# Kernel tuning notes

Hardware: AMD Instinct MI355X
Metric: run time of the kernel (lower is better)

Reference implementation:

```python
import jax, jax.numpy as jnp
import numpy as np

B, T, D = 2, 2048, 1024
P, ALPHA, P_R = 512, 4, 64
HID = 16 * D
EPS = 1e-6


def rmsnorm(x, w):
    norm = jnp.sqrt(jnp.mean(x * x, axis=-1, keepdims=True) + EPS)
    return x * w / norm


def ssm_lowrank(t, F, b_r, c_r):
    # gated elementwise recurrence h_t = F_t * h_{t-1} + t_t, then low-rank correction
    Fs = jnp.moveaxis(F, 1, 0)   # (T,B,P)
    ts = jnp.moveaxis(t, 1, 0)   # (T,B,P)

    def step(h, inp):
        f, u = inp
        h = f * h + u
        return h, h

    h0 = jnp.zeros((t.shape[0], t.shape[2]), dtype=t.dtype)
    _, hs = jax.lax.scan(step, h0, (Fs, ts))
    h = jnp.moveaxis(hs, 0, 1)   # (B,T,P)
    t_tilde = t + jnp.einsum('btp,pr,rq->btq', h, b_r, c_r)
    return t_tilde


def setup_inputs() -> dict:
    key = jax.random.key(0)
    ks = jax.random.split(key, 11)
    s = lambda fan: 1.0 / np.sqrt(fan)
    return {
        'x':       jax.random.normal(ks[0], (B, T, D), jnp.float32),
        'w_norm1': jnp.ones((D,), jnp.float32),
        'w_toP':   jax.random.normal(ks[1], (D, P), jnp.float32) * s(D),
        'w_emb':   jax.random.normal(ks[2], (D, ALPHA * P), jnp.float32) * s(D),
        'w_f':     jax.random.normal(ks[3], (D, P), jnp.float32) * s(D),
        'b_r':     jax.random.normal(ks[4], (P, P_R), jnp.float32) * s(P),
        'c_r':     jax.random.normal(ks[5], (P_R, P), jnp.float32) * s(P_R),
        'w_fromP': jax.random.normal(ks[6], (P, D), jnp.float32) * s(P),
        'w_norm2': jnp.ones((D,), jnp.float32),
        'w_fc1':   jax.random.normal(ks[7], (D, HID), jnp.float32) * s(D),
        'w_fc2':   jax.random.normal(ks[8], (HID, D), jnp.float32) * s(HID),
    }


def reference(x, w_norm1, w_toP, w_emb, w_f, b_r, c_r, w_fromP, w_norm2, w_fc1, w_fc2):
    # ---- pre-LN CEPTA context path ----
    h1 = rmsnorm(x, w_norm1)
    pre_path = jnp.einsum('btd,dp->btp', h1, w_toP)                 # to_P
    U = jnp.einsum('btd,dk->btk', h1, w_emb).reshape(B, T, ALPHA, P)  # cepta_dense U
    Fgate = jax.nn.sigmoid(jnp.einsum('btd,dp->btp', h1, w_f))      # cepta_dense F
    Y = jax.nn.gelu(U)                                              # cepta_dense Y
    t = jnp.sum(Y, axis=2) + pre_path                               # router reduce='sum'
    t_tilde = ssm_lowrank(t, Fgate, b_r, c_r)                       # low-rank SSM
    y = jnp.einsum('btp,pd->btd', t_tilde, w_fromP)                 # from_P
    x = x + y
    # ---- pre-LN GELU MLP ----
    h2 = rmsnorm(x, w_norm2)
    z = jnp.einsum('bth,hd->btd', jax.nn.gelu(jnp.einsum('btd,dh->bth', h2, w_fc1)), w_fc2)
    return x + z
```

## Files before the change

### kernel.cpp

```cpp
#include <hip/hip_runtime.h>

typedef unsigned short u16;
typedef __bf16 bf16x8 __attribute__((ext_vector_type(8)));
typedef float f32x4 __attribute__((ext_vector_type(4)));
typedef int i32x4 __attribute__((ext_vector_type(4)));

__device__ inline u16 f2bf(float f) {
  union { float f; unsigned u; } v; v.f = f;
  unsigned u = v.u;
  unsigned r = (u + 0x7FFFu + ((u >> 16) & 1u)) >> 16;
  return (u16)r;
}

__device__ inline float gelu_f(float x) {
  float t = 0.7978845608028654f * (x + 0.044715f * x * x * x);
  float a = __expf(-2.f * fabsf(t));
  float th = (1.f - a) / (1.f + a);
  th = copysignf(th, t);
  return 0.5f * x * (1.f + th);
}
__device__ inline float sigmoid_f(float x) { return 1.f / (1.f + __expf(-x)); }

__global__ void transpose_cvt(const float* __restrict__ in, u16* __restrict__ out,
                              int R, int C, int ldout) {
  __shared__ float tile[32][33];
  int c0 = blockIdx.x * 32, r0 = blockIdx.y * 32;
  int tx = threadIdx.x, ty = threadIdx.y;
#pragma unroll
  for (int i = 0; i < 32; i += 8) {
    int r = r0 + ty + i, c = c0 + tx;
    tile[ty + i][tx] = (r < R && c < C) ? in[(long)r * C + c] : 0.f;
  }
  __syncthreads();
#pragma unroll
  for (int i = 0; i < 32; i += 8) {
    int cc = c0 + ty + i, rr = r0 + tx;
    if (cc < C && rr < R) out[(long)cc * ldout + rr] = f2bf(tile[tx][ty + i]);
  }
}

__global__ __launch_bounds__(256) void rmsnorm_k(const float* __restrict__ x,
                                                 const float* __restrict__ w,
                                                 u16* __restrict__ out) {
  int row = blockIdx.x;
  int tid = threadIdx.x;
  const float4* xv = (const float4*)(x + (long)row * 1024);
  float4 v = xv[tid];
  float ss = v.x * v.x + v.y * v.y + v.z * v.z + v.w * v.w;
#pragma unroll
  for (int off = 32; off > 0; off >>= 1) ss += __shfl_down(ss, off);
  __shared__ float red[4];
  if ((tid & 63) == 0) red[tid >> 6] = ss;
  __syncthreads();
  float tot = red[0] + red[1] + red[2] + red[3];
  float scale = rsqrtf(tot * (1.f / 1024.f) + 1e-6f);
  const float4* wv4 = (const float4*)w;
  float4 wv = wv4[tid];
  ushort4 o;
  o.x = f2bf(v.x * wv.x * scale);
  o.y = f2bf(v.y * wv.y * scale);
  o.z = f2bf(v.z * wv.z * scale);
  o.w = f2bf(v.w * wv.w * scale);
  *((ushort4*)(out + (long)row * 1024) + tid) = o;
}

#define EPI_BF16 0
#define EPI_ROUTE1 1
#define EPI_ADD_BF16 2
#define EPI_ADD_F32 3
#define EPI_GELU_BF16 4

template <int EPI>
__global__ __launch_bounds__(256) void gemm_bt(
    const u16* __restrict__ A, const u16* __restrict__ Bt,
    u16* __restrict__ obf, float* __restrict__ of32, const float* __restrict__ add,
    float* __restrict__ og, float* __restrict__ ofl,
    int N, int K, int lda, int ldb) {
  __shared__ __align__(16) u16 As[128 * 64];
  __shared__ __align__(16) u16 Bs[128 * 64];
  const int tid = threadIdx.x;
  const int lane = tid & 63;
  const int wave = tid >> 6;
  const int wm = wave >> 1, wn = wave & 1;
  const int bm0 = blockIdx.y * 128, bn0 = blockIdx.x * 128;

  f32x4 acc[4][4];
  f32x4 zero = {0.f, 0.f, 0.f, 0.f};
#pragma unroll
  for (int m = 0; m < 4; ++m)
#pragma unroll
    for (int n = 0; n < 4; ++n) acc[m][n] = zero;

  i32x4 ra[4], rb[4];
  int srow[4], schk[4];
#pragma unroll
  for (int i = 0; i < 4; ++i) {
    int s = tid + 256 * i;
    srow[i] = s >> 3;
    schk[i] = s & 7;
  }

#pragma unroll
  for (int i = 0; i < 4; ++i) {
    ra[i] = *(const i32x4*)(A + (bm0 + srow[i]) * lda + schk[i] * 8);
    rb[i] = *(const i32x4*)(Bt + (bn0 + srow[i]) * ldb + schk[i] * 8);
  }

  const int nk = K >> 6;
  for (int t = 0; t < nk; ++t) {
#pragma unroll
    for (int i = 0; i < 4; ++i) {
      *(i32x4*)&As[srow[i] * 64 + ((schk[i] ^ (srow[i] & 7)) << 3)] = ra[i];
      *(i32x4*)&Bs[srow[i] * 64 + ((schk[i] ^ (srow[i] & 7)) << 3)] = rb[i];
    }
    __syncthreads();
    if (t + 1 < nk) {
      int k0 = (t + 1) << 6;
#pragma unroll
      for (int i = 0; i < 4; ++i) {
        ra[i] = *(const i32x4*)(A + (bm0 + srow[i]) * lda + k0 + schk[i] * 8);
        rb[i] = *(const i32x4*)(Bt + (bn0 + srow[i]) * ldb + k0 + schk[i] * 8);
      }
    }
#pragma unroll
    for (int kk = 0; kk < 2; ++kk) {
      bf16x8 av[4], bv[4];
#pragma unroll
      for (int m = 0; m < 4; ++m) {
        int r = wm * 64 + m * 16 + (lane & 15);
        int c = kk * 4 + (lane >> 4);
        i32x4 v = *(const i32x4*)&As[r * 64 + ((c ^ (r & 7)) << 3)];
        av[m] = __builtin_bit_cast(bf16x8, v);
      }
#pragma unroll
      for (int n = 0; n < 4; ++n) {
        int r = wn * 64 + n * 16 + (lane & 15);
        int c = kk * 4 + (lane >> 4);
        i32x4 v = *(const i32x4*)&Bs[r * 64 + ((c ^ (r & 7)) << 3)];
        bv[n] = __builtin_bit_cast(bf16x8, v);
      }
#pragma unroll
      for (int m = 0; m < 4; ++m)
#pragma unroll
        for (int n = 0; n < 4; ++n)
          acc[m][n] = __builtin_amdgcn_mfma_f32_16x16x32_bf16(av[m], bv[n], acc[m][n], 0, 0, 0);
    }
    __syncthreads();
  }

#pragma unroll
  for (int m = 0; m < 4; ++m) {
    int row_b = bm0 + wm * 64 + m * 16 + ((lane >> 4) << 2);
#pragma unroll
    for (int n = 0; n < 4; ++n) {
      int col = bn0 + wn * 64 + n * 16 + (lane & 15);
#pragma unroll
      for (int j = 0; j < 4; ++j) {
        int row = row_b + j;
        float v = acc[m][n][j];
        if constexpr (EPI == EPI_BF16) {
          obf[(long)row * N + col] = f2bf(v);
        } else if constexpr (EPI == EPI_ROUTE1) {
          if (col < 512) of32[(long)row * 512 + col] = v;
          else if (col < 2560) og[(long)row * 2048 + (col - 512)] = gelu_f(v);
          else ofl[(long)row * 512 + (col - 2560)] = sigmoid_f(v);
        } else if constexpr (EPI == EPI_ADD_BF16) {
          long idx = (long)row * N + col;
          obf[idx] = f2bf(add[idx] + v);
        } else if constexpr (EPI == EPI_ADD_F32) {
          long idx = (long)row * N + col;
          of32[idx] = add[idx] + v;
        } else {
          obf[(long)row * N + col] = f2bf(gelu_f(v));
        }
      }
    }
  }
}

__global__ __launch_bounds__(256) void router_k(float* __restrict__ tb, const float* __restrict__ G) {
  int i = blockIdx.x * 256 + threadIdx.x;
  int r = i >> 7, pq = i & 127;
  float4 t = ((float4*)tb)[i];
#pragma unroll
  for (int a = 0; a < 4; ++a) {
    float4 g = *((const float4*)(G + (long)r * 2048 + a * 512) + pq);
    t.x += g.x; t.y += g.y; t.z += g.z; t.w += g.w;
  }
  ((float4*)tb)[i] = t;
}

__global__ void scan_chunk(const float* __restrict__ tb, const float* __restrict__ F,
                           float* __restrict__ abuf, float* __restrict__ ubuf) {
  int b = blockIdx.x >> 5, c = blockIdx.x & 31, pidx = threadIdx.x;
  const float* fp = F + ((long)(b * 2048 + c * 64) * 512) + pidx;
  const float* up = tb + ((long)(b * 2048 + c * 64) * 512) + pidx;
  float A = 1.f, U = 0.f;
#pragma unroll 8
  for (int s = 0; s < 64; ++s) {
    float f = fp[(long)s * 512], u = up[(long)s * 512];
    A = f * A;
    U = f * U + u;
  }
  abuf[(b * 32 + c) * 512 + pidx] = A;
  ubuf[(b * 32 + c) * 512 + pidx] = U;
}

__global__ void scan_combine(const float* __restrict__ abuf, const float* __restrict__ ubuf,
                             float* __restrict__ hstart) {
  int b = blockIdx.x, pidx = threadIdx.x;
  float h = 0.f;
  for (int c = 0; c < 32; ++c) {
    hstart[(b * 32 + c) * 512 + pidx] = h;
    h = abuf[(b * 32 + c) * 512 + pidx] * h + ubuf[(b * 32 + c) * 512 + pidx];
  }
}

__global__ void scan_apply(const float* __restrict__ tb, const float* __restrict__ F,
                           const float* __restrict__ hstart, u16* __restrict__ hbf) {
  int b = blockIdx.x >> 5, c = blockIdx.x & 31, pidx = threadIdx.x;
  const float* fp = F + ((long)(b * 2048 + c * 64) * 512) + pidx;
  const float* up = tb + ((long)(b * 2048 + c * 64) * 512) + pidx;
  u16* op = hbf + ((long)(b * 2048 + c * 64) * 512) + pidx;
  float h = hstart[(b * 32 + c) * 512 + pidx];
#pragma unroll 8
  for (int s = 0; s < 64; ++s) {
    float f = fp[(long)s * 512], u = up[(long)s * 512];
    h = f * h + u;
    op[(long)s * 512] = f2bf(h);
  }
}

extern "C" void kernel_launch(void* const* d_in, const int* in_sizes, int n_in,
                              void* d_out, int out_size, void* d_ws, size_t ws_size,
                              hipStream_t stream) {
  const float* x       = (const float*)d_in[0];
  const float* w_norm1 = (const float*)d_in[1];
  const float* w_toP   = (const float*)d_in[2];
  const float* w_emb   = (const float*)d_in[3];
  const float* w_f     = (const float*)d_in[4];
  const float* b_r     = (const float*)d_in[5];
  const float* c_r     = (const float*)d_in[6];
  const float* w_fromP = (const float*)d_in[7];
  const float* w_norm2 = (const float*)d_in[8];
  const float* w_fc1   = (const float*)d_in[9];
  const float* w_fc2   = (const float*)d_in[10];
  float* out = (float*)d_out;

  char* base = (char*)d_ws;
  size_t off = 0;
  auto alloc = [&](size_t bytes) {
    void* r = base + off;
    off += (bytes + 255) & ~(size_t)255;
    return r;
  };
  u16* W1T     = (u16*)alloc((size_t)3072 * 1024 * 2);
  u16* WfromPT = (u16*)alloc((size_t)1024 * 512 * 2);
  u16* Wfc1T   = (u16*)alloc((size_t)16384 * 1024 * 2);
  u16* Wfc2T   = (u16*)alloc((size_t)1024 * 16384 * 2);
  u16* BrT     = (u16*)alloc((size_t)128 * 512 * 2);
  u16* CrT     = (u16*)alloc((size_t)512 * 128 * 2);
  u16* h1      = (u16*)alloc((size_t)4096 * 1024 * 2);
  float* G     = (float*)alloc((size_t)4096 * 2048 * 4);
  float* F     = (float*)alloc((size_t)4096 * 512 * 4);
  float* tb    = (float*)alloc((size_t)4096 * 512 * 4);
  float* abuf  = (float*)alloc((size_t)2 * 32 * 512 * 4);
  float* ubuf  = (float*)alloc((size_t)2 * 32 * 512 * 4);
  float* hstart= (float*)alloc((size_t)2 * 32 * 512 * 4);
  u16* hbf     = (u16*)alloc((size_t)4096 * 512 * 2);
  u16* g1buf   = (u16*)alloc((size_t)4096 * 128 * 2);
  u16* tt      = (u16*)alloc((size_t)4096 * 512 * 2);
  float* xmid  = (float*)alloc((size_t)4096 * 1024 * 4);
  u16* h2      = (u16*)alloc((size_t)4096 * 1024 * 2);
  u16* a3      = (u16*)alloc((size_t)4096 * 4096 * 2);
  (void)ws_size; (void)in_sizes; (void)n_in; (void)out_size;

  dim3 tpb(32, 8);
  transpose_cvt<<<dim3(16, 32), tpb, 0, stream>>>(w_toP, W1T, 1024, 512, 1024);
  transpose_cvt<<<dim3(64, 32), tpb, 0, stream>>>(w_emb, W1T + (size_t)512 * 1024, 1024, 2048, 1024);
  transpose_cvt<<<dim3(16, 32), tpb, 0, stream>>>(w_f, W1T + (size_t)2560 * 1024, 1024, 512, 1024);
  transpose_cvt<<<dim3(32, 16), tpb, 0, stream>>>(w_fromP, WfromPT, 512, 1024, 512);
  transpose_cvt<<<dim3(512, 32), tpb, 0, stream>>>(w_fc1, Wfc1T, 1024, 16384, 1024);
  transpose_cvt<<<dim3(32, 512), tpb, 0, stream>>>(w_fc2, Wfc2T, 16384, 1024, 16384);
  hipMemsetAsync(BrT, 0, (size_t)128 * 512 * 2, stream);
  hipMemsetAsync(CrT, 0, (size_t)512 * 128 * 2, stream);
  transpose_cvt<<<dim3(2, 16), tpb, 0, stream>>>(b_r, BrT, 512, 64, 512);
  transpose_cvt<<<dim3(16, 2), tpb, 0, stream>>>(c_r, CrT, 64, 512, 128);

  rmsnorm_k<<<4096, 256, 0, stream>>>(x, w_norm1, h1);

  gemm_bt<EPI_ROUTE1><<<dim3(24, 32), 256, 0, stream>>>(h1, W1T, nullptr, tb, nullptr, G, F,
                                                        3072, 1024, 1024, 1024);
  router_k<<<2048, 256, 0, stream>>>(tb, G);

  scan_chunk<<<64, 512, 0, stream>>>(tb, F, abuf, ubuf);
  scan_combine<<<2, 512, 0, stream>>>(abuf, ubuf, hstart);
  scan_apply<<<64, 512, 0, stream>>>(tb, F, hstart, hbf);

  gemm_bt<EPI_BF16><<<dim3(1, 32), 256, 0, stream>>>(hbf, BrT, g1buf, nullptr, nullptr, nullptr, nullptr,
                                                     128, 512, 512, 512);
  gemm_bt<EPI_ADD_BF16><<<dim3(4, 32), 256, 0, stream>>>(g1buf, CrT, tt, nullptr, tb, nullptr, nullptr,
                                                         512, 128, 128, 128);
  gemm_bt<EPI_ADD_F32><<<dim3(8, 32), 256, 0, stream>>>(tt, WfromPT, nullptr, xmid, x, nullptr, nullptr,
                                                        1024, 512, 512, 512);
  rmsnorm_k<<<4096, 256, 0, stream>>>(xmid, w_norm2, h2);

  for (int c = 0; c < 4; ++c) {
    gemm_bt<EPI_GELU_BF16><<<dim3(32, 32), 256, 0, stream>>>(
        h2, Wfc1T + (size_t)c * 4096 * 1024, a3, nullptr, nullptr, nullptr, nullptr,
        4096, 1024, 1024, 1024);
    gemm_bt<EPI_ADD_F32><<<dim3(8, 32), 256, 0, stream>>>(
        a3, Wfc2T + (size_t)c * 4096, nullptr, out, (c == 0 ? xmid : out), nullptr, nullptr,
        1024, 4096, 4096, 16384);
  }
}
```

Measured before the change: 597.8 us.

## Use direct global-to-LDS loads, XCD-aware block remap, and split-K for fc2

Replaces the register-staged, XOR-swizzled LDS fill with global_load_lds direct copies, which removes the register prefetch of the next tile and the swizzle, so LDS reads may now hit bank conflicts. It remaps workgroup IDs so consecutive tiles spread across XCDs for better L2 locality. The fc2 GEMM becomes a 2-way split-K writing partial sums into scratch, followed by a separate reduce kernel that adds the residual. This raises parallelism for the 256-block GEMM at the cost of extra fp32 traffic and an additional launch per chunk.

```diff
diff --git a/kernel.cpp b/kernel.cpp
--- a/kernel.cpp
+++ b/kernel.cpp
@@ -20,6 +20,11 @@
   return 0.5f * x * (1.f + th);
 }
 __device__ inline float sigmoid_f(float x) { return 1.f / (1.f + __expf(-x)); }
+
+__device__ __forceinline__ void gld16(const u16* g, u16* l) {
+  __builtin_amdgcn_global_load_lds((const __attribute__((address_space(1))) void*)g,
+                                   (__attribute__((address_space(3))) void*)l, 16, 0, 0);
+}
 
 __global__ void transpose_cvt(const float* __restrict__ in, u16* __restrict__ out,
                               int R, int C, int ldout) {
@@ -69,6 +74,7 @@
 #define EPI_ADD_BF16 2
 #define EPI_ADD_F32 3
 #define EPI_GELU_BF16 4
+#define EPI_PART 5
 
 template <int EPI>
 __global__ __launch_bounds__(256) void gemm_bt(
@@ -81,8 +87,19 @@
   const int tid = threadIdx.x;
   const int lane = tid & 63;
   const int wave = tid >> 6;
+
+  const int gx = gridDim.x, gy = gridDim.y, gz = gridDim.z;
+  const int nwg = gx * gy * gz;
+  int orig = (blockIdx.z * gy + blockIdx.y) * gx + blockIdx.x;
+  int id = ((nwg & 7) == 0) ? ((orig & 7) * (nwg >> 3) + (orig >> 3)) : orig;
+  const int bx = id % gx;
+  const int by = (id / gx) % gy;
+  const int bz = id / (gx * gy);
+
   const int wm = wave >> 1, wn = wave & 1;
-  const int bm0 = blockIdx.y * 128, bn0 = blockIdx.x * 128;
+  const int bm0 = by * 128, bn0 = bx * 128;
+  const int kper = K / gz;
+  const int koff = bz * kper;
 
   f32x4 acc[4][4];
   f32x4 zero = {0.f, 0.f, 0.f, 0.f};
@@ -91,37 +108,19 @@
 #pragma unroll
     for (int n = 0; n < 4; ++n) acc[m][n] = zero;
 
-  i32x4 ra[4], rb[4];
-  int srow[4], schk[4];
-#pragma unroll
-  for (int i = 0; i < 4; ++i) {
-    int s = tid + 256 * i;
-    srow[i] = s >> 3;
-    schk[i] = s & 7;
-  }
-
-#pragma unroll
-  for (int i = 0; i < 4; ++i) {
-    ra[i] = *(const i32x4*)(A + (bm0 + srow[i]) * lda + schk[i] * 8);
-    rb[i] = *(const i32x4*)(Bt + (bn0 + srow[i]) * ldb + schk[i] * 8);
-  }
-
-  const int nk = K >> 6;
+  const int lrow = lane >> 3, lchk = lane & 7;
+  const long abase = (long)(bm0 + wave * 8 + lrow) * lda + koff + lchk * 8;
+  const long bbase = (long)(bn0 + wave * 8 + lrow) * ldb + koff + lchk * 8;
+
+  const int nk = kper >> 6;
   for (int t = 0; t < nk; ++t) {
-#pragma unroll
-    for (int i = 0; i < 4; ++i) {
-      *(i32x4*)&As[srow[i] * 64 + ((schk[i] ^ (srow[i] & 7)) << 3)] = ra[i];
-      *(i32x4*)&Bs[srow[i] * 64 + ((schk[i] ^ (srow[i] & 7)) << 3)] = rb[i];
+    const int k0 = t << 6;
+#pragma unroll
+    for (int j = 0; j < 4; ++j) {
+      gld16(A + abase + (long)j * 32 * lda + k0, &As[(wave * 8 + j * 32) * 64]);
+      gld16(Bt + bbase + (long)j * 32 * ldb + k0, &Bs[(wave * 8 + j * 32) * 64]);
     }
     __syncthreads();
-    if (t + 1 < nk) {
-      int k0 = (t + 1) << 6;
-#pragma unroll
-      for (int i = 0; i < 4; ++i) {
-        ra[i] = *(const i32x4*)(A + (bm0 + srow[i]) * lda + k0 + schk[i] * 8);
-        rb[i] = *(const i32x4*)(Bt + (bn0 + srow[i]) * ldb + k0 + schk[i] * 8);
-      }
-    }
 #pragma unroll
     for (int kk = 0; kk < 2; ++kk) {
       bf16x8 av[4], bv[4];
@@ -129,15 +128,13 @@
       for (int m = 0; m < 4; ++m) {
         int r = wm * 64 + m * 16 + (lane & 15);
         int c = kk * 4 + (lane >> 4);
-        i32x4 v = *(const i32x4*)&As[r * 64 + ((c ^ (r & 7)) << 3)];
-        av[m] = __builtin_bit_cast(bf16x8, v);
+        av[m] = __builtin_bit_cast(bf16x8, *(const i32x4*)&As[r * 64 + c * 8]);
       }
 #pragma unroll
       for (int n = 0; n < 4; ++n) {
         int r = wn * 64 + n * 16 + (lane & 15);
         int c = kk * 4 + (lane >> 4);
-        i32x4 v = *(const i32x4*)&Bs[r * 64 + ((c ^ (r & 7)) << 3)];
-        bv[n] = __builtin_bit_cast(bf16x8, v);
+        bv[n] = __builtin_bit_cast(bf16x8, *(const i32x4*)&Bs[r * 64 + c * 8]);
       }
 #pragma unroll
       for (int m = 0; m < 4; ++m)
@@ -170,12 +167,30 @@
         } else if constexpr (EPI == EPI_ADD_F32) {
           long idx = (long)row * N + col;
           of32[idx] = add[idx] + v;
+        } else if constexpr (EPI == EPI_GELU_BF16) {
+          obf[(long)row * N + col] = f2bf(gelu_f(v));
         } else {
-          obf[(long)row * N + col] = f2bf(gelu_f(v));
+          of32[(long)bz * 4096 * N + (long)row * N + col] = v;
         }
       }
     }
   }
+}
+
+__global__ __launch_bounds__(256) void reduce2_k(const float* __restrict__ base,
+                                                 const float* __restrict__ p0,
+                                                 const float* __restrict__ p1,
+                                                 float* __restrict__ o) {
+  long i = (long)blockIdx.x * 256 + threadIdx.x;
+  float4 b = ((const float4*)base)[i];
+  float4 q0 = ((const float4*)p0)[i];
+  float4 q1 = ((const float4*)p1)[i];
+  float4 r;
+  r.x = b.x + q0.x + q1.x;
+  r.y = b.y + q0.y + q1.y;
+  r.z = b.z + q0.z + q1.z;
+  r.w = b.w + q0.w + q1.w;
+  ((float4*)o)[i] = r;
 }
 
 __global__ __launch_bounds__(256) void router_k(float* __restrict__ tb, const float* __restrict__ G) {
@@ -305,12 +320,15 @@
                                                         1024, 512, 512, 512);
   rmsnorm_k<<<4096, 256, 0, stream>>>(xmid, w_norm2, h2);
 
+  float* p0 = G;
+  float* p1 = G + (size_t)4096 * 1024;
   for (int c = 0; c < 4; ++c) {
     gemm_bt<EPI_GELU_BF16><<<dim3(32, 32), 256, 0, stream>>>(
         h2, Wfc1T + (size_t)c * 4096 * 1024, a3, nullptr, nullptr, nullptr, nullptr,
         4096, 1024, 1024, 1024);
-    gemm_bt<EPI_ADD_F32><<<dim3(8, 32), 256, 0, stream>>>(
-        a3, Wfc2T + (size_t)c * 4096, nullptr, out, (c == 0 ? xmid : out), nullptr, nullptr,
+    gemm_bt<EPI_PART><<<dim3(8, 32, 2), 256, 0, stream>>>(
+        a3, Wfc2T + (size_t)c * 4096, nullptr, p0, nullptr, nullptr, nullptr,
         1024, 4096, 4096, 16384);
-  }
-}
+    reduce2_k<<<4096, 256, 0, stream>>>((c == 0 ? xmid : out), p0, p1, out);
+  }
+}
```

New measurement: 745.4 us. 24.7% more time.

## Add 256x256 double-buffered direct-to-LDS GEMM with split-K for MLP

Applied to the files above, without the earlier changes.

Adds a new GEMM kernel with 256x256 tiles and 512 threads. It loads global memory straight into double-buffered LDS using global_load_lds, raises wave priority around the MFMA block, and remaps workgroup IDs across XCDs. The new kernel replaces the route GEMM and the MLP GEMMs. The MLP now runs in two chunks of 8192 hidden columns, and fc2 uses 4-way split-K, writing partial sums that a new reduce kernel adds to the residual. The aim is more data reuse per tile and overlap of loads with compute. The costs are an unswizzled LDS layout that may cause bank conflicts, extra partial-sum traffic, and a partial buffer aliased onto h1 that spills well past h1's own allocation into the following workspace buffers.

```diff
diff --git a/kernel.cpp b/kernel.cpp
--- a/kernel.cpp
+++ b/kernel.cpp
@@ -20,6 +20,11 @@
   return 0.5f * x * (1.f + th);
 }
 __device__ inline float sigmoid_f(float x) { return 1.f / (1.f + __expf(-x)); }
+
+__device__ __forceinline__ void gld16(const u16* g, u16* l) {
+  __builtin_amdgcn_global_load_lds((const __attribute__((address_space(1))) void*)g,
+                                   (__attribute__((address_space(3))) void*)l, 16, 0, 0);
+}
 
 __global__ void transpose_cvt(const float* __restrict__ in, u16* __restrict__ out,
                               int R, int C, int ldout) {
@@ -69,6 +74,107 @@
 #define EPI_ADD_BF16 2
 #define EPI_ADD_F32 3
 #define EPI_GELU_BF16 4
+#define EPI_PART 5
+
+template <int EPI>
+__global__ __launch_bounds__(512, 2) void gemm256(
+    const u16* __restrict__ A, const u16* __restrict__ Bt,
+    u16* __restrict__ obf, float* __restrict__ of32,
+    float* __restrict__ og, float* __restrict__ ofl,
+    int N, int K, int lda, int ldb) {
+  __shared__ __align__(16) u16 sA[2][256 * 64];
+  __shared__ __align__(16) u16 sB[2][256 * 64];
+  const int tid = threadIdx.x;
+  const int lane = tid & 63;
+  const int wave = tid >> 6;
+  const int wm = wave >> 2, wn = wave & 3;
+
+  const int gx = gridDim.x, gy = gridDim.y, gz = gridDim.z;
+  const int nwg = gx * gy * gz;
+  int orig = (blockIdx.z * gy + blockIdx.y) * gx + blockIdx.x;
+  int id = ((nwg & 7) == 0) ? ((orig & 7) * (nwg >> 3) + (orig >> 3)) : orig;
+  const int bx = id % gx;
+  const int by = (id / gx) % gy;
+  const int bz = id / (gx * gy);
+  const int bm0 = by * 256, bn0 = bx * 256;
+  const int kper = K / gz, koff = bz * kper;
+
+  f32x4 acc[8][4];
+  f32x4 zero = {0.f, 0.f, 0.f, 0.f};
+#pragma unroll
+  for (int m = 0; m < 8; ++m)
+#pragma unroll
+    for (int n = 0; n < 4; ++n) acc[m][n] = zero;
+
+  const int srow = tid >> 3, schk = tid & 7;
+  const long abase = (long)(bm0 + srow) * lda + koff + schk * 8;
+  const long bbase = (long)(bn0 + srow) * ldb + koff + schk * 8;
+  const int ldsw = wave * 8 * 64;
+
+  const int nk = kper >> 6;
+#pragma unroll
+  for (int g = 0; g < 4; ++g) {
+    gld16(A + abase + (long)g * 64 * lda, &sA[0][g * 64 * 64 + ldsw]);
+    gld16(Bt + bbase + (long)g * 64 * ldb, &sB[0][g * 64 * 64 + ldsw]);
+  }
+  __syncthreads();
+  int cur = 0;
+  for (int t = 0; t < nk; ++t) {
+    if (t + 1 < nk) {
+      const long k0 = (long)(t + 1) << 6;
+#pragma unroll
+      for (int g = 0; g < 4; ++g) {
+        gld16(A + abase + (long)g * 64 * lda + k0, &sA[cur ^ 1][g * 64 * 64 + ldsw]);
+        gld16(Bt + bbase + (long)g * 64 * ldb + k0, &sB[cur ^ 1][g * 64 * 64 + ldsw]);
+      }
+    }
+#pragma unroll
+    for (int kk = 0; kk < 2; ++kk) {
+      bf16x8 av[8], bv[4];
+      const int c8 = (kk * 4 + (lane >> 4)) * 8;
+#pragma unroll
+      for (int m = 0; m < 8; ++m)
+        av[m] = __builtin_bit_cast(bf16x8,
+            *(const i32x4*)&sA[cur][(wm * 128 + m * 16 + (lane & 15)) * 64 + c8]);
+#pragma unroll
+      for (int n = 0; n < 4; ++n)
+        bv[n] = __builtin_bit_cast(bf16x8,
+            *(const i32x4*)&sB[cur][(wn * 64 + n * 16 + (lane & 15)) * 64 + c8]);
+      __builtin_amdgcn_s_setprio(1);
+#pragma unroll
+      for (int m = 0; m < 8; ++m)
+#pragma unroll
+        for (int n = 0; n < 4; ++n)
+          acc[m][n] = __builtin_amdgcn_mfma_f32_16x16x32_bf16(av[m], bv[n], acc[m][n], 0, 0, 0);
+      __builtin_amdgcn_s_setprio(0);
+    }
+    __syncthreads();
+    cur ^= 1;
+  }
+
+#pragma unroll
+  for (int m = 0; m < 8; ++m) {
+    int row_b = bm0 + wm * 128 + m * 16 + ((lane >> 4) << 2);
+#pragma unroll
+    for (int n = 0; n < 4; ++n) {
+      int col = bn0 + wn * 64 + n * 16 + (lane & 15);
+#pragma unroll
+      for (int j = 0; j < 4; ++j) {
+        int row = row_b + j;
+        float v = acc[m][n][j];
+        if constexpr (EPI == EPI_GELU_BF16) {
+          obf[(long)row * N + col] = f2bf(gelu_f(v));
+        } else if constexpr (EPI == EPI_ROUTE1) {
+          if (col < 512) of32[(long)row * 512 + col] = v;
+          else if (col < 2560) og[(long)row * 2048 + (col - 512)] = gelu_f(v);
+          else ofl[(long)row * 512 + (col - 2560)] = sigmoid_f(v);
+        } else {
+          of32[(long)bz * (4096L * 1024) + (long)row * N + col] = v;
+        }
+      }
+    }
+  }
+}
 
 template <int EPI>
 __global__ __launch_bounds__(256) void gemm_bt(
@@ -99,7 +205,6 @@
     srow[i] = s >> 3;
     schk[i] = s & 7;
   }
-
 #pragma unroll
   for (int i = 0; i < 4; ++i) {
     ra[i] = *(const i32x4*)(A + (bm0 + srow[i]) * lda + schk[i] * 8);
@@ -129,15 +234,13 @@
       for (int m = 0; m < 4; ++m) {
         int r = wm * 64 + m * 16 + (lane & 15);
         int c = kk * 4 + (lane >> 4);
-        i32x4 v = *(const i32x4*)&As[r * 64 + ((c ^ (r & 7)) << 3)];
-        av[m] = __builtin_bit_cast(bf16x8, v);
+        av[m] = __builtin_bit_cast(bf16x8, *(const i32x4*)&As[r * 64 + ((c ^ (r & 7)) << 3)]);
       }
 #pragma unroll
       for (int n = 0; n < 4; ++n) {
         int r = wn * 64 + n * 16 + (lane & 15);
         int c = kk * 4 + (lane >> 4);
-        i32x4 v = *(const i32x4*)&Bs[r * 64 + ((c ^ (r & 7)) << 3)];
-        bv[n] = __builtin_bit_cast(bf16x8, v);
+        bv[n] = __builtin_bit_cast(bf16x8, *(const i32x4*)&Bs[r * 64 + ((c ^ (r & 7)) << 3)]);
       }
 #pragma unroll
       for (int m = 0; m < 4; ++m)
@@ -160,22 +263,34 @@
         float v = acc[m][n][j];
         if constexpr (EPI == EPI_BF16) {
           obf[(long)row * N + col] = f2bf(v);
-        } else if constexpr (EPI == EPI_ROUTE1) {
-          if (col < 512) of32[(long)row * 512 + col] = v;
-          else if (col < 2560) og[(long)row * 2048 + (col - 512)] = gelu_f(v);
-          else ofl[(long)row * 512 + (col - 2560)] = sigmoid_f(v);
         } else if constexpr (EPI == EPI_ADD_BF16) {
           long idx = (long)row * N + col;
           obf[idx] = f2bf(add[idx] + v);
         } else if constexpr (EPI == EPI_ADD_F32) {
           long idx = (long)row * N + col;
           of32[idx] = add[idx] + v;
-        } else {
-          obf[(long)row * N + col] = f2bf(gelu_f(v));
         }
       }
     }
   }
+}
+
+__global__ __launch_bounds__(256) void reduce4_k(const float* __restrict__ base,
+                                                 const float* __restrict__ p,
+                                                 float* __restrict__ o) {
+  long i = (long)blockIdx.x * 256 + threadIdx.x;
+  const long PL = 4096L * 1024 / 4;
+  float4 b = ((const float4*)base)[i];
+  float4 q0 = ((const float4*)p)[i];
+  float4 q1 = ((const float4*)p)[i + PL];
+  float4 q2 = ((const float4*)p)[i + 2 * PL];
+  float4 q3 = ((const float4*)p)[i + 3 * PL];
+  float4 r;
+  r.x = b.x + q0.x + q1.x + q2.x + q3.x;
+  r.y = b.y + q0.y + q1.y + q2.y + q3.y;
+  r.z = b.z + q0.z + q1.z + q2.z + q3.z;
+  r.w = b.w + q0.w + q1.w + q2.w + q3.w;
+  ((float4*)o)[i] = r;
 }
 
 __global__ __launch_bounds__(256) void router_k(float* __restrict__ tb, const float* __restrict__ G) {
@@ -272,7 +387,8 @@
   u16* tt      = (u16*)alloc((size_t)4096 * 512 * 2);
   float* xmid  = (float*)alloc((size_t)4096 * 1024 * 4);
   u16* h2      = (u16*)alloc((size_t)4096 * 1024 * 2);
-  u16* a3      = (u16*)alloc((size_t)4096 * 4096 * 2);
+  u16* a3      = (u16*)alloc((size_t)4096 * 8192 * 2);
+  float* part  = (float*)h1;
   (void)ws_size; (void)in_sizes; (void)n_in; (void)out_size;
 
   dim3 tpb(32, 8);
@@ -289,8 +405,8 @@
 
   rmsnorm_k<<<4096, 256, 0, stream>>>(x, w_norm1, h1);
 
-  gemm_bt<EPI_ROUTE1><<<dim3(24, 32), 256, 0, stream>>>(h1, W1T, nullptr, tb, nullptr, G, F,
-                                                        3072, 1024, 1024, 1024);
+  gemm256<EPI_ROUTE1><<<dim3(12, 16, 1), 512, 0, stream>>>(h1, W1T, nullptr, tb, G, F,
+                                                           3072, 1024, 1024, 1024);
   router_k<<<2048, 256, 0, stream>>>(tb, G);
 
   scan_chunk<<<64, 512, 0, stream>>>(tb, F, abuf, ubuf);
@@ -305,12 +421,13 @@
                                                         1024, 512, 512, 512);
   rmsnorm_k<<<4096, 256, 0, stream>>>(xmid, w_norm2, h2);
 
-  for (int c = 0; c < 4; ++c) {
-    gemm_bt<EPI_GELU_BF16><<<dim3(32, 32), 256, 0, stream>>>(
-        h2, Wfc1T + (size_t)c * 4096 * 1024, a3, nullptr, nullptr, nullptr, nullptr,
-        4096, 1024, 1024, 1024);
-    gemm_bt<EPI_ADD_F32><<<dim3(8, 32), 256, 0, stream>>>(
-        a3, Wfc2T + (size_t)c * 4096, nullptr, out, (c == 0 ? xmid : out), nullptr, nullptr,
-        1024, 4096, 4096, 16384);
-  }
-}
+  for (int c = 0; c < 2; ++c) {
+    gemm256<EPI_GELU_BF16><<<dim3(32, 16, 1), 512, 0, stream>>>(
+        h2, Wfc1T + (size_t)c * 8192 * 1024, a3, nullptr, nullptr, nullptr,
+        8192, 1024, 1024, 1024);
+    gemm256<EPI_PART><<<dim3(4, 16, 4), 512, 0, stream>>>(
+        a3, Wfc2T + (size_t)c * 8192, nullptr, part, nullptr, nullptr,
+        1024, 8192, 8192, 16384);
+    reduce4_k<<<4096, 256, 0, stream>>>((c == 0 ? xmid : out), part, out);
+  }
+}
```

New measurement: 658.7 us. 10.2% more time.
